# Performance work log

Hardware: AMD Instinct MI355X
Metric: run time of the kernel (lower is better)

## Reference

```python
import jax, jax.numpy as jnp
import numpy as np

B, T, F = 32, 2048, 64  # projection_dim must equal feature_dim for the original forward to type-check
SCALE = float(np.sqrt(F))


def setup_inputs() -> dict:
    key = jax.random.key(0)
    k_x, k_q, k_k = jax.random.split(key, 3)
    x = jax.random.normal(k_x, (B, T, F), dtype=jnp.float32)
    # torch nn.Linear weight is (out_features, in_features); y = x @ W.T
    lim = 1.0 / np.sqrt(F)
    W_q = jax.random.uniform(k_q, (F, F), dtype=jnp.float32, minval=-lim, maxval=lim)
    W_k = jax.random.uniform(k_k, (F, F), dtype=jnp.float32, minval=-lim, maxval=lim)
    gamma = jnp.zeros((1, 1, F), dtype=jnp.float32)
    return {"x": x, "W_q": W_q, "W_k": W_k, "gamma": gamma}


def reference(x, W_q, W_k, gamma):
    # Q, K: (B,T,F) -- Linear without bias: x @ W.T
    Q = jnp.einsum('btf,pf->btp', x, W_q)
    K = jnp.einsum('btf,pf->btp', x, W_k)
    # per-timestep outer product: scores[b,t,i,j] = Q[b,t,i]*K[b,t,j]/scale -> (B,T,F,F)
    scores = Q[..., :, None] * K[..., None, :] / SCALE
    attn_weights = jax.nn.softmax(scores, axis=-1)
    # mixed[b,t,i] = sum_j attn[b,t,i,j] * x[b,t,j]
    mixed = jnp.einsum('btij,btj->bti', attn_weights, x)
    out = x + gamma * mixed
    return (out, attn_weights)
```

## Files before the change

kernel.cpp:

```cpp
#include <hip/hip_runtime.h>


#define LOG2E 1.4426950408889634f

constexpr int F = 64;

typedef _Float16 h2v __attribute__((ext_vector_type(2)));

#if defined(__has_builtin)
#if __has_builtin(__builtin_amdgcn_fdot2)
#define HAVE_FDOT2 1
#endif
#endif

static __device__ __forceinline__ float fdot2(h2v a, h2v b, float c) {
#ifdef HAVE_FDOT2
    return __builtin_amdgcn_fdot2(a, b, c, false);
#else
    return c + (float)a[0] * (float)b[0] + (float)a[1] * (float)b[1];
#endif
}

__global__ __launch_bounds__(256, 4)
void fsattn(const float* __restrict__ X,
            const float* __restrict__ Wq,
            const float* __restrict__ Wk,
            const float* __restrict__ gamma,
            float* __restrict__ out,
            float* __restrict__ attn,
            int BT)
{
    const int lane = threadIdx.x & 63;
    const int wid  = threadIdx.x >> 6;
    const int gw   = (blockIdx.x << 2) + wid;
    const int nw   = gridDim.x << 2;

    __shared__ float    x_lds[4][F];
    __shared__ float    k_lds[4][F];
    __shared__ _Float16 xh_lds[4][F];
    __shared__ float2   ql_lds[4][F];

    h2v wq2[32], wk2[32];
#pragma unroll
    for (int p = 0; p < 32; ++p) {
        const float2 a = reinterpret_cast<const float2*>(Wq + lane * F)[p];
        const float2 b = reinterpret_cast<const float2*>(Wk + lane * F)[p];
        h2v ha; ha[0] = (_Float16)a.x; ha[1] = (_Float16)a.y;
        h2v hb; hb[0] = (_Float16)b.x; hb[1] = (_Float16)b.y;
        wq2[p] = ha; wk2[p] = hb;
    }
    const float g = gamma[lane];

    for (int t = gw; t < BT; t += nw) {
        const float xv = X[(size_t)t * F + lane];
        x_lds[wid][lane]  = xv;
        xh_lds[wid][lane] = (_Float16)xv;
        __builtin_amdgcn_wave_barrier();

        float q = 0.f, k = 0.f;
        const h2v* xh = reinterpret_cast<const h2v*>(xh_lds[wid]);
#pragma unroll
        for (int p = 0; p < 32; ++p) {
            const h2v xp = xh[p];
            q = fdot2(wq2[p], xp, q);
            k = fdot2(wk2[p], xp, k);
        }
        const float qs = q * (0.125f * LOG2E);
        k_lds[wid][lane] = k;
        __builtin_amdgcn_wave_barrier();

        float sum0 = 0.f, sum1 = 0.f, mix0 = 0.f, mix1 = 0.f;
#pragma unroll
        for (int j = 0; j < 16; ++j) {
            const float4 k4 = reinterpret_cast<const float4*>(k_lds[wid])[j];
            const float4 x4 = reinterpret_cast<const float4*>(x_lds[wid])[j];
            const float e0 = __builtin_amdgcn_exp2f(qs * k4.x);
            const float e1 = __builtin_amdgcn_exp2f(qs * k4.y);
            const float e2 = __builtin_amdgcn_exp2f(qs * k4.z);
            const float e3 = __builtin_amdgcn_exp2f(qs * k4.w);
            sum0 += e0 + e1;
            sum1 += e2 + e3;
            mix0 = __builtin_fmaf(e0, x4.x, __builtin_fmaf(e1, x4.y, mix0));
            mix1 = __builtin_fmaf(e2, x4.z, __builtin_fmaf(e3, x4.w, mix1));
        }
        const float sum = sum0 + sum1;
        const float inv = __builtin_amdgcn_rcpf(sum);
        const float li  = -__builtin_amdgcn_logf(sum);
        float2 ql; ql.x = qs; ql.y = li;
        ql_lds[wid][lane] = ql;
        __builtin_amdgcn_wave_barrier();

        out[(size_t)t * F + lane] = xv + g * ((mix0 + mix1) * inv);

        float* ap = attn + (size_t)t * (F * F);
        const int sub = lane >> 4;
        const int c16 = lane & 15;
        const float4 kc = reinterpret_cast<const float4*>(k_lds[wid])[c16];
#pragma unroll
        for (int i0 = 0; i0 < F; i0 += 4) {
            const int row = i0 + sub;
            const float2 qr = ql_lds[wid][row];
            float4 w;
            w.x = __builtin_amdgcn_exp2f(__builtin_fmaf(qr.x, kc.x, qr.y));
            w.y = __builtin_amdgcn_exp2f(__builtin_fmaf(qr.x, kc.y, qr.y));
            w.z = __builtin_amdgcn_exp2f(__builtin_fmaf(qr.x, kc.z, qr.y));
            w.w = __builtin_amdgcn_exp2f(__builtin_fmaf(qr.x, kc.w, qr.y));
            reinterpret_cast<float4*>(ap + (size_t)row * F)[c16] = w;
        }
    }
}

extern "C" void kernel_launch(void* const* d_in, const int* in_sizes, int n_in,
                              void* d_out, int out_size, void* d_ws, size_t ws_size,
                              hipStream_t stream) {
    const float* X     = (const float*)d_in[0];
    const float* Wq    = (const float*)d_in[1];
    const float* Wk    = (const float*)d_in[2];
    const float* gamma = (const float*)d_in[3];

    const int BT = in_sizes[0] / F;
    float* out  = (float*)d_out;
    float* attn = out + (size_t)BT * F;

    dim3 grid(1024), block(256);
    hipLaunchKernelGGL(fsattn, grid, block, 0, stream,
                       X, Wq, Wk, gamma, out, attn, BT);
}
```

Baseline: 227.1 us.

## Software-pipeline timesteps: prefetch next x and interleave prior attn stores

Restructures the per-wave timestep loop into a software pipeline with double-buffered LDS. The next timestep's x is prefetched from global memory one iteration ahead, and the attention-weight writes for the previous timestep are interleaved with the softmax-sum loop of the current one, so memory stores overlap with exp/FMA work. It also merges the split sum/mix accumulators into single chains. This adds register pressure, doubles LDS per wave, and needs prologue and epilogue code.

Result: slower. 382.3 us (+68.3%).

```diff
diff --git a/kernel.cpp b/kernel.cpp
--- a/kernel.cpp
+++ b/kernel.cpp
@@ -35,10 +35,10 @@
     const int gw   = (blockIdx.x << 2) + wid;
     const int nw   = gridDim.x << 2;
 
-    __shared__ float    x_lds[4][F];
-    __shared__ float    k_lds[4][F];
-    __shared__ _Float16 xh_lds[4][F];
-    __shared__ float2   ql_lds[4][F];
+    __shared__ float    x_lds[4][2][F];
+    __shared__ _Float16 xh_lds[4][2][F];
+    __shared__ float    k_lds[4][2][F];
+    __shared__ float2   ql_lds[4][2][F];
 
     h2v wq2[32], wk2[32];
 #pragma unroll
@@ -50,15 +50,21 @@
         wq2[p] = ha; wk2[p] = hb;
     }
     const float g = gamma[lane];
+    const int sub = lane >> 4;
+    const int c16 = lane & 15;
 
-    for (int t = gw; t < BT; t += nw) {
-        const float xv = X[(size_t)t * F + lane];
-        x_lds[wid][lane]  = xv;
-        xh_lds[wid][lane] = (_Float16)xv;
+    if (gw >= BT) return;
+
+    int buf = 0;
+    int tprev = gw;
+    float xv = X[(size_t)gw * F + lane];
+    float xnext = (gw + nw < BT) ? X[(size_t)(gw + nw) * F + lane] : 0.f;
+    {
+        x_lds[wid][0][lane]  = xv;
+        xh_lds[wid][0][lane] = (_Float16)xv;
         __builtin_amdgcn_wave_barrier();
-
         float q = 0.f, k = 0.f;
-        const h2v* xh = reinterpret_cast<const h2v*>(xh_lds[wid]);
+        const h2v* xh = reinterpret_cast<const h2v*>(xh_lds[wid][0]);
 #pragma unroll
         for (int p = 0; p < 32; ++p) {
             const h2v xp = xh[p];
@@ -66,40 +72,93 @@
             k = fdot2(wk2[p], xp, k);
         }
         const float qs = q * (0.125f * LOG2E);
-        k_lds[wid][lane] = k;
+        k_lds[wid][0][lane] = k;
         __builtin_amdgcn_wave_barrier();
 
-        float sum0 = 0.f, sum1 = 0.f, mix0 = 0.f, mix1 = 0.f;
+        float sum = 0.f, mix = 0.f;
 #pragma unroll
         for (int j = 0; j < 16; ++j) {
-            const float4 k4 = reinterpret_cast<const float4*>(k_lds[wid])[j];
-            const float4 x4 = reinterpret_cast<const float4*>(x_lds[wid])[j];
+            const float4 k4 = reinterpret_cast<const float4*>(k_lds[wid][0])[j];
+            const float4 x4 = reinterpret_cast<const float4*>(x_lds[wid][0])[j];
             const float e0 = __builtin_amdgcn_exp2f(qs * k4.x);
             const float e1 = __builtin_amdgcn_exp2f(qs * k4.y);
             const float e2 = __builtin_amdgcn_exp2f(qs * k4.z);
             const float e3 = __builtin_amdgcn_exp2f(qs * k4.w);
-            sum0 += e0 + e1;
-            sum1 += e2 + e3;
-            mix0 = __builtin_fmaf(e0, x4.x, __builtin_fmaf(e1, x4.y, mix0));
-            mix1 = __builtin_fmaf(e2, x4.z, __builtin_fmaf(e3, x4.w, mix1));
+            sum += (e0 + e1) + (e2 + e3);
+            mix = __builtin_fmaf(e0, x4.x, __builtin_fmaf(e1, x4.y,
+                  __builtin_fmaf(e2, x4.z, __builtin_fmaf(e3, x4.w, mix))));
         }
-        const float sum = sum0 + sum1;
         const float inv = __builtin_amdgcn_rcpf(sum);
         const float li  = -__builtin_amdgcn_logf(sum);
         float2 ql; ql.x = qs; ql.y = li;
-        ql_lds[wid][lane] = ql;
+        ql_lds[wid][0][lane] = ql;
+        __builtin_amdgcn_wave_barrier();
+        out[(size_t)gw * F + lane] = xv + g * (mix * inv);
+    }
+
+    for (int t = gw + nw; t < BT; t += nw) {
+        const int nbuf = buf ^ 1;
+        xv = xnext;
+        xnext = (t + nw < BT) ? X[(size_t)(t + nw) * F + lane] : 0.f;
+
+        x_lds[wid][nbuf][lane]  = xv;
+        xh_lds[wid][nbuf][lane] = (_Float16)xv;
+        __builtin_amdgcn_wave_barrier();
+        float q = 0.f, k = 0.f;
+        const h2v* xh = reinterpret_cast<const h2v*>(xh_lds[wid][nbuf]);
+#pragma unroll
+        for (int p = 0; p < 32; ++p) {
+            const h2v xp = xh[p];
+            q = fdot2(wq2[p], xp, q);
+            k = fdot2(wk2[p], xp, k);
+        }
+        const float qs = q * (0.125f * LOG2E);
+        k_lds[wid][nbuf][lane] = k;
         __builtin_amdgcn_wave_barrier();
 
-        out[(size_t)t * F + lane] = xv + g * ((mix0 + mix1) * inv);
+        float* ap = attn + (size_t)tprev * (F * F);
+        const float4 kc = reinterpret_cast<const float4*>(k_lds[wid][buf])[c16];
+        float sum = 0.f, mix = 0.f;
+#pragma unroll
+        for (int j = 0; j < 16; ++j) {
+            const float4 k4 = reinterpret_cast<const float4*>(k_lds[wid][nbuf])[j];
+            const float4 x4 = reinterpret_cast<const float4*>(x_lds[wid][nbuf])[j];
+            const float e0 = __builtin_amdgcn_exp2f(qs * k4.x);
+            const float e1 = __builtin_amdgcn_exp2f(qs * k4.y);
+            const float e2 = __builtin_amdgcn_exp2f(qs * k4.z);
+            const float e3 = __builtin_amdgcn_exp2f(qs * k4.w);
+            sum += (e0 + e1) + (e2 + e3);
+            mix = __builtin_fmaf(e0, x4.x, __builtin_fmaf(e1, x4.y,
+                  __builtin_fmaf(e2, x4.z, __builtin_fmaf(e3, x4.w, mix))));
 
-        float* ap = attn + (size_t)t * (F * F);
-        const int sub = lane >> 4;
-        const int c16 = lane & 15;
-        const float4 kc = reinterpret_cast<const float4*>(k_lds[wid])[c16];
+            const int row = 4 * j + sub;
+            const float2 qr = ql_lds[wid][buf][row];
+            float4 w;
+            w.x = __builtin_amdgcn_exp2f(__builtin_fmaf(qr.x, kc.x, qr.y));
+            w.y = __builtin_amdgcn_exp2f(__builtin_fmaf(qr.x, kc.y, qr.y));
+            w.z = __builtin_amdgcn_exp2f(__builtin_fmaf(qr.x, kc.z, qr.y));
+            w.w = __builtin_amdgcn_exp2f(__builtin_fmaf(qr.x, kc.w, qr.y));
+            reinterpret_cast<float4*>(ap + (size_t)row * F)[c16] = w;
+        }
+
+        const float inv = __builtin_amdgcn_rcpf(sum);
+        const float li  = -__builtin_amdgcn_logf(sum);
+        float2 ql; ql.x = qs; ql.y = li;
+        ql_lds[wid][nbuf][lane] = ql;
+        __builtin_amdgcn_wave_barrier();
+        out[(size_t)t * F + lane] = xv + g * (mix * inv);
+
+        tprev = t;
+        buf = nbuf;
+    }
+
+    {
+        float* ap = attn + (size_t)tprev * (F * F);
+        const float4 kc = reinterpret_cast<const float4*>(k_lds[wid][buf])[c16];
 #pragma unroll
-        for (int i0 = 0; i0 < F; i0 += 4) {
-            const int row = i0 + sub;
-            const float2 qr = ql_lds[wid][row];
+        for (int j = 0; j < 16; ++j) {
+            const int row = 4 * j + sub;
+            const float2 qr = ql_lds[wid][buf][row];
             float4 w;
             w.x = __builtin_amdgcn_exp2f(__builtin_fmaf(qr.x, kc.x, qr.y));
             w.y = __builtin_amdgcn_exp2f(__builtin_fmaf(qr.x, kc.y, qr.y));
```

## Split into Q/K projection kernel and row-parallel softmax-write kernel

Applied to the files above, without the earlier changes.

Splits the fused kernel into two launches. The first computes Q and K into a workspace buffer. The second assigns each wave one group of four attention rows, computes exp, row sums via shuffles and the mixed output, and prefetches the next chunk's operands into registers. The aim is higher occupancy and better write throughput on the dominant attention-output stream, and it removes the recomputation of exp and log for normalization. The costs are an extra launch, a round trip through workspace memory for Q and K, and redundant per-row exp work. The original monolithic kernel is kept as a fallback when the workspace is too small.

Measured after the change: 392.4 us. 72.7% more time.

```diff
diff --git a/kernel.cpp b/kernel.cpp
--- a/kernel.cpp
+++ b/kernel.cpp
@@ -22,13 +22,124 @@
 }
 
 __global__ __launch_bounds__(256, 4)
-void fsattn(const float* __restrict__ X,
-            const float* __restrict__ Wq,
-            const float* __restrict__ Wk,
-            const float* __restrict__ gamma,
-            float* __restrict__ out,
-            float* __restrict__ attn,
-            int BT)
+void fsattn_qk(const float* __restrict__ X,
+               const float* __restrict__ Wq,
+               const float* __restrict__ Wk,
+               float* __restrict__ kbuf,
+               float* __restrict__ qsbuf,
+               int BT)
+{
+    const int lane = threadIdx.x & 63;
+    const int wid  = threadIdx.x >> 6;
+    const int gw   = (blockIdx.x << 2) + wid;
+    const int nw   = gridDim.x << 2;
+
+    __shared__ _Float16 xh_lds[4][F];
+
+    h2v wq2[32], wk2[32];
+#pragma unroll
+    for (int p = 0; p < 32; ++p) {
+        const float2 a = reinterpret_cast<const float2*>(Wq + lane * F)[p];
+        const float2 b = reinterpret_cast<const float2*>(Wk + lane * F)[p];
+        h2v ha; ha[0] = (_Float16)a.x; ha[1] = (_Float16)a.y;
+        h2v hb; hb[0] = (_Float16)b.x; hb[1] = (_Float16)b.y;
+        wq2[p] = ha; wk2[p] = hb;
+    }
+
+    for (int t = gw; t < BT; t += nw) {
+        const float xv = X[(size_t)t * F + lane];
+        xh_lds[wid][lane] = (_Float16)xv;
+        __builtin_amdgcn_wave_barrier();
+
+        float q = 0.f, k = 0.f;
+        const h2v* xh = reinterpret_cast<const h2v*>(xh_lds[wid]);
+#pragma unroll
+        for (int p = 0; p < 32; ++p) {
+            const h2v xp = xh[p];
+            q = fdot2(wq2[p], xp, q);
+            k = fdot2(wk2[p], xp, k);
+        }
+        __builtin_amdgcn_wave_barrier();
+
+        kbuf [(size_t)t * F + lane] = k;
+        qsbuf[(size_t)t * F + lane] = q * (0.125f * LOG2E);
+    }
+}
+
+__global__ __launch_bounds__(256, 8)
+void fsattn_wr(const float* __restrict__ X,
+               const float* __restrict__ kbuf,
+               const float* __restrict__ qsbuf,
+               const float* __restrict__ gamma,
+               float* __restrict__ out,
+               float* __restrict__ attn,
+               long NC)
+{
+    const int lane = threadIdx.x & 63;
+    const int c16  = lane & 15;
+    const int sub  = lane >> 4;
+    const long gwv = (long)((blockIdx.x * blockDim.x + threadIdx.x) >> 6);
+    const long nwv = (long)((gridDim.x * blockDim.x) >> 6);
+
+    long c = gwv;
+    if (c >= NC) return;
+
+    int t   = (int)(c >> 4);
+    int row = ((int)(c & 15)) * 4 + sub;
+    float4 kc  = reinterpret_cast<const float4*>(kbuf + (size_t)t * F)[c16];
+    float4 x4  = reinterpret_cast<const float4*>(X    + (size_t)t * F)[c16];
+    float  qsr = qsbuf[(size_t)t * F + row];
+    float  xr  = X    [(size_t)t * F + row];
+    float  gr  = gamma[row];
+
+    for (; c < NC; c += nwv) {
+        const long cn = c + nwv;
+        const float4 kcc = kc;  const float4 x4c = x4;
+        const float  qsc = qsr; const float  xrc = xr; const float grc = gr;
+        const int    tc  = t;   const int    rowc = row;
+
+        if (cn < NC) {
+            t   = (int)(cn >> 4);
+            row = ((int)(cn & 15)) * 4 + sub;
+            kc  = reinterpret_cast<const float4*>(kbuf + (size_t)t * F)[c16];
+            x4  = reinterpret_cast<const float4*>(X    + (size_t)t * F)[c16];
+            qsr = qsbuf[(size_t)t * F + row];
+            xr  = X    [(size_t)t * F + row];
+            gr  = gamma[row];
+        }
+
+        const float e0 = __builtin_amdgcn_exp2f(qsc * kcc.x);
+        const float e1 = __builtin_amdgcn_exp2f(qsc * kcc.y);
+        const float e2 = __builtin_amdgcn_exp2f(qsc * kcc.z);
+        const float e3 = __builtin_amdgcn_exp2f(qsc * kcc.w);
+
+        float ps = (e0 + e1) + (e2 + e3);
+        float pm = __builtin_fmaf(e0, x4c.x, __builtin_fmaf(e1, x4c.y,
+                   __builtin_fmaf(e2, x4c.z, e3 * x4c.w)));
+#pragma unroll
+        for (int s = 1; s < 16; s <<= 1) {
+            ps += __shfl_xor(ps, s, 64);
+            pm += __shfl_xor(pm, s, 64);
+        }
+        const float inv = __builtin_amdgcn_rcpf(ps);
+
+        float4 w;
+        w.x = e0 * inv; w.y = e1 * inv; w.z = e2 * inv; w.w = e3 * inv;
+        reinterpret_cast<float4*>(attn + (size_t)c * 256)[lane] = w;
+
+        if (c16 == 0)
+            out[(size_t)tc * F + rowc] = xrc + grc * (pm * inv);
+    }
+}
+
+__global__ __launch_bounds__(256, 4)
+void fsattn_mono(const float* __restrict__ X,
+                 const float* __restrict__ Wq,
+                 const float* __restrict__ Wk,
+                 const float* __restrict__ gamma,
+                 float* __restrict__ out,
+                 float* __restrict__ attn,
+                 int BT)
 {
     const int lane = threadIdx.x & 63;
     const int wid  = threadIdx.x >> 6;
@@ -122,7 +233,17 @@
     float* out  = (float*)d_out;
     float* attn = out + (size_t)BT * F;
 
-    dim3 grid(1024), block(256);
-    hipLaunchKernelGGL(fsattn, grid, block, 0, stream,
-                       X, Wq, Wk, gamma, out, attn, BT);
-}
+    const size_t need = 2ull * (size_t)BT * F * sizeof(float);
+    if (ws_size >= need) {
+        float* kbuf  = (float*)d_ws;
+        float* qsbuf = kbuf + (size_t)BT * F;
+        hipLaunchKernelGGL(fsattn_qk, dim3(1024), dim3(256), 0, stream,
+                           X, Wq, Wk, kbuf, qsbuf, BT);
+        const long NC = (long)BT * 16;
+        hipLaunchKernelGGL(fsattn_wr, dim3(2048), dim3(256), 0, stream,
+                           X, kbuf, qsbuf, gamma, out, attn, NC);
+    } else {
+        hipLaunchKernelGGL(fsattn_mono, dim3(1024), dim3(256), 0, stream,
+                           X, Wq, Wk, gamma, out, attn, BT);
+    }
+}
```
